# Kernel tuning notes

Hardware: AMD Instinct MI355X
Metric: run time of the kernel (lower is better)

## Reference

```python
import jax, jax.numpy as jnp
import numpy as np

N_NODES = 50000
N_EDGES = 800000
NUM_GRAPHS = 128
FEAT = 128
HID = 64
NUM_LAYERS = 3
OUT = 2
K = 30
LATENT = HID * NUM_LAYERS + 1  # 193 = conv1 kernel size & stride


def _lin(k, i, o):
    s = 1.0 / np.sqrt(i)
    return jax.random.uniform(k, (i, o), jnp.float32, -s, s)


def setup_inputs() -> dict:
    key = jax.random.key(0)
    ks = jax.random.split(key, 16)
    x = jax.random.normal(ks[0], (N_NODES, FEAT), jnp.float32)
    edge_index = jax.random.randint(ks[1], (2, N_EDGES), 0, N_NODES, dtype=jnp.int64)
    batch = jnp.sort(jax.random.randint(ks[2], (N_NODES,), 0, NUM_GRAPHS, dtype=jnp.int64))
    w0 = _lin(ks[3], FEAT, HID); b0 = jnp.zeros((HID,), jnp.float32)
    w1 = _lin(ks[4], HID, HID);  b1 = jnp.zeros((HID,), jnp.float32)
    w2 = _lin(ks[5], HID, HID);  b2 = jnp.zeros((HID,), jnp.float32)
    w3 = _lin(ks[6], HID, 1);    b3 = jnp.zeros((1,), jnp.float32)
    conv1_w = jax.random.normal(ks[7], (16, 1, LATENT), jnp.float32) * (1.0 / np.sqrt(LATENT))
    conv1_b = jnp.zeros((16,), jnp.float32)
    conv2_w = jax.random.normal(ks[8], (32, 16, 5), jnp.float32) * (1.0 / np.sqrt(16 * 5))
    conv2_b = jnp.zeros((32,), jnp.float32)
    dense_dim = (int((K - 2) / 2 + 1) - 5 + 1) * 32  # 352
    lin1_w = _lin(ks[9], dense_dim, 256); lin1_b = jnp.zeros((256,), jnp.float32)
    lin2_w = _lin(ks[10], 256, OUT);      lin2_b = jnp.zeros((OUT,), jnp.float32)
    return dict(x=x, edge_index=edge_index, batch=batch,
                w0=w0, b0=b0, w1=w1, b1=b1, w2=w2, b2=b2, w3=w3, b3=b3,
                conv1_w=conv1_w, conv1_b=conv1_b, conv2_w=conv2_w, conv2_b=conv2_b,
                lin1_w=lin1_w, lin1_b=lin1_b, lin2_w=lin2_w, lin2_b=lin2_b)


def _gcn(h_in, w, b, src, dst, norm, n):
    # GCNConv: out_i = sum_j d_i^-1/2 d_j^-1/2 (x_j W) over A+I, plus bias
    h = h_in @ w
    msg = h[src] * norm[:, None]  # gather over edges (incl. self loops)
    return jax.ops.segment_sum(msg, dst, num_segments=n) + b


def _sort_pool(x, batch, k, g):
    # per-graph descending sort on last channel, top-k, zero-pad
    n, d = x.shape
    order = jnp.lexsort((-x[:, -1], batch))  # primary: batch asc, secondary: last feat desc
    xs, bs = x[order], batch[order]
    counts = jax.ops.segment_sum(jnp.ones((n,), jnp.int32), batch, num_segments=g)
    starts = jnp.cumsum(counts) - counts
    rank = jnp.arange(n) - starts[bs]
    slot = jnp.where(rank < k, rank, k)  # overflow nodes dumped in slot k (discarded)
    out = jnp.zeros((g, k + 1, d), x.dtype).at[bs, slot].set(xs)
    return out[:, :k].reshape(g, k * d)


def _conv1d(z, w, stride):
    return jax.lax.conv_general_dilated(z, w, window_strides=(stride,), padding='VALID',
                                        dimension_numbers=('NCH', 'OIH', 'NCH'))


def reference(x, edge_index, batch, w0, b0, w1, b1, w2, b2, w3, b3,
              conv1_w, conv1_b, conv2_w, conv2_b, lin1_w, lin1_b, lin2_w, lin2_b):
    n = x.shape[0]
    loop = jnp.arange(n, dtype=edge_index.dtype)
    src = jnp.concatenate([edge_index[0], loop])
    dst = jnp.concatenate([edge_index[1], loop])
    deg = jax.ops.segment_sum(jnp.ones_like(src, jnp.float32), dst, num_segments=n)
    dinv = jnp.where(deg > 0, jax.lax.rsqrt(deg), 0.0)
    norm = dinv[src] * dinv[dst]

    h1 = jnp.tanh(_gcn(x,  w0, b0, src, dst, norm, n))
    h2 = jnp.tanh(_gcn(h1, w1, b1, src, dst, norm, n))
    h3 = jnp.tanh(_gcn(h2, w2, b2, src, dst, norm, n))
    h4 = jnp.tanh(_gcn(h3, w3, b3, src, dst, norm, n))
    hcat = jnp.concatenate([h1, h2, h3, h4], axis=-1)  # [N, 193]

    p = _sort_pool(hcat, batch, K, NUM_GRAPHS)  # [G, K*193]
    z = p[:, None, :]                                   # [G, 1, K*193]
    z = jax.nn.relu(_conv1d(z, conv1_w, LATENT) + conv1_b[None, :, None])  # [G,16,K]
    g, c, l = z.shape
    z = z.reshape(g, c, l // 2, 2).max(axis=-1)         # MaxPool1d(2,2) -> [G,16,15]
    z = jax.nn.relu(_conv1d(z, conv2_w, 1) + conv2_b[None, :, None])       # [G,32,11]
    z = z.reshape(g, -1)                                # [G,352]
    z = jax.nn.relu(z @ lin1_w + lin1_b)
    # dropout is identity in eval mode
    return z @ lin2_w + lin2_b
```

## Files before the change

### kernel.cpp

```cpp
#include <hip/hip_runtime.h>
#include <math.h>

#define NGRAPH 128
#define KTOP 30
#define LATENT 193
#define HID 64

typedef unsigned short u16;

__global__ void k_zero(int* edeg, int n) {
    int i = blockIdx.x * blockDim.x + threadIdx.x;
    if (i < n) edeg[i] = 0;
}

__global__ __launch_bounds__(256) void k_gemm_hist(
        const float* __restrict__ A, const float* __restrict__ W,
        float* __restrict__ Hs, int M, int K, int NG,
        const int* __restrict__ dst, const int* __restrict__ batch,
        int* edeg, u16* __restrict__ rank, int* starts,
        int E, int n) {
    __shared__ float As[64][17];
    __shared__ float Bs[16][65];
    int bid = blockIdx.x;
    int gemm_id = (bid % 5 == 0) ? bid / 5 : -1;
    if (gemm_id >= 0 && gemm_id < NG) {
        int tid = threadIdx.x;
        int tx = tid & 15, ty = tid >> 4;
        int br = gemm_id * 64;
        float c[4][4] = {};
        for (int k0 = 0; k0 < K; k0 += 16) {
            {
                int idx = tid * 4;
                int r = idx >> 4;
                int kk = idx & 15;
                int grow = br + r;
                float4 v = make_float4(0.f, 0.f, 0.f, 0.f);
                if (grow < M) v = *(const float4*)(A + (size_t)grow * K + k0 + kk);
                As[r][kk + 0] = v.x; As[r][kk + 1] = v.y;
                As[r][kk + 2] = v.z; As[r][kk + 3] = v.w;
            }
            {
                int idx = tid * 4;
                int kk = idx >> 6;
                int col = idx & 63;
                float4 v = *(const float4*)(W + (size_t)(k0 + kk) * 64 + col);
                Bs[kk][col + 0] = v.x; Bs[kk][col + 1] = v.y;
                Bs[kk][col + 2] = v.z; Bs[kk][col + 3] = v.w;
            }
            __syncthreads();
#pragma unroll
            for (int kk = 0; kk < 16; ++kk) {
                float a[4], b[4];
#pragma unroll
                for (int i = 0; i < 4; i++) a[i] = As[ty + i * 16][kk];
#pragma unroll
                for (int j = 0; j < 4; j++) b[j] = Bs[kk][tx + j * 16];
#pragma unroll
                for (int i = 0; i < 4; i++)
#pragma unroll
                    for (int j = 0; j < 4; j++) c[i][j] += a[i] * b[j];
            }
            __syncthreads();
        }
#pragma unroll
        for (int i = 0; i < 4; i++) {
            int row = br + ty + i * 16;
            if (row >= M) continue;
#pragma unroll
            for (int j = 0; j < 4; j++) {
                int col = tx + j * 16;
                Hs[(size_t)row * HID + col] = c[i][j];
            }
        }
    } else {
        int ngb = min((bid + 4) / 5, NG);
        int fid = bid - ngb;
        int gi = fid * 256 + threadIdx.x;
        if (gi < n) {
            int b = batch[gi];
            if (gi == 0) {
                for (int g = 0; g <= b; g++) starts[g] = 0;
            } else {
                int pb = batch[gi - 1];
                for (int g = pb + 1; g <= b; g++) starts[g] = gi;
            }
            if (gi == n - 1) {
                for (int g = b + 1; g <= NGRAPH; g++) starts[g] = n;
            }
        }
        if (gi < E) {
            int d = dst[gi];
            rank[gi] = (u16)atomicAdd(&edeg[d], 1);
        }
    }
}

__global__ void k_scan1(const int* __restrict__ edeg, int* offs, int* bsum,
                        float* dinv, int n) {
    __shared__ int s[256];
    int t = threadIdx.x;
    int gi = blockIdx.x * 256 + t;
    int v = (gi < n) ? edeg[gi] : 0;
    if (gi < n) dinv[gi] = rsqrtf((float)(v + 1));
    s[t] = v;
    __syncthreads();
    for (int o = 1; o < 256; o <<= 1) {
        int add = (t >= o) ? s[t - o] : 0;
        __syncthreads();
        s[t] += add;
        __syncthreads();
    }
    if (gi < n) offs[gi] = s[t] - v;
    if (t == 255) bsum[blockIdx.x] = s[255];
}

__global__ void k_scan23(int* offs, const int* __restrict__ bsum,
                         int n, int E, int nb) {
    __shared__ int s[256];
    int t = threadIdx.x;
    int bid = blockIdx.x;
    int v = (t < nb) ? bsum[t] : 0;
    s[t] = v;
    __syncthreads();
    for (int o = 1; o < 256; o <<= 1) {
        int add = (t >= o) ? s[t - o] : 0;
        __syncthreads();
        s[t] += add;
        __syncthreads();
    }
    int boffv = (bid == 0) ? 0 : s[bid - 1];
    int gi = bid * 256 + t;
    if (gi < n) offs[gi] += boffv;
    if (gi == 0) offs[n] = E;
}

__global__ __launch_bounds__(256) void k_fill(const int* __restrict__ src,
                                              const int* __restrict__ dst,
                                              const u16* __restrict__ rank,
                                              const int* __restrict__ offs,
                                              u16* __restrict__ csr, int E) {
    int t = blockIdx.x * 256 + threadIdx.x;
    int e0 = t * 4;
    if (e0 + 4 <= E) {
        int4 s4 = *(const int4*)(src + e0);
        int4 d4 = *(const int4*)(dst + e0);
        const u16* rp = rank + e0;
        csr[offs[d4.x] + rp[0]] = (u16)s4.x;
        csr[offs[d4.y] + rp[1]] = (u16)s4.y;
        csr[offs[d4.z] + rp[2]] = (u16)s4.z;
        csr[offs[d4.w] + rp[3]] = (u16)s4.w;
    } else {
        for (int e = e0; e < E; e++)
            csr[offs[dst[e]] + rank[e]] = (u16)src[e];
    }
}

__global__ __launch_bounds__(256) void k_gemm(const float* __restrict__ A,
                                              const float* __restrict__ W,
                                              const float* __restrict__ dinv,
                                              float* __restrict__ Hs,
                                              int M, int K) {
    __shared__ float As[64][17];
    __shared__ float Bs[16][65];
    int tid = threadIdx.x;
    int tx = tid & 15, ty = tid >> 4;
    int br = blockIdx.x * 64;
    float c[4][4] = {};
    for (int k0 = 0; k0 < K; k0 += 16) {
        {
            int idx = tid * 4;
            int r = idx >> 4;
            int kk = idx & 15;
            int grow = br + r;
            float4 v = make_float4(0.f, 0.f, 0.f, 0.f);
            if (grow < M) v = *(const float4*)(A + (size_t)grow * K + k0 + kk);
            As[r][kk + 0] = v.x; As[r][kk + 1] = v.y;
            As[r][kk + 2] = v.z; As[r][kk + 3] = v.w;
        }
        {
            int idx = tid * 4;
            int kk = idx >> 6;
            int col = idx & 63;
            float4 v = *(const float4*)(W + (size_t)(k0 + kk) * 64 + col);
            Bs[kk][col + 0] = v.x; Bs[kk][col + 1] = v.y;
            Bs[kk][col + 2] = v.z; Bs[kk][col + 3] = v.w;
        }
        __syncthreads();
#pragma unroll
        for (int kk = 0; kk < 16; ++kk) {
            float a[4], b[4];
#pragma unroll
            for (int i = 0; i < 4; i++) a[i] = As[ty + i * 16][kk];
#pragma unroll
            for (int j = 0; j < 4; j++) b[j] = Bs[kk][tx + j * 16];
#pragma unroll
            for (int i = 0; i < 4; i++)
#pragma unroll
                for (int j = 0; j < 4; j++) c[i][j] += a[i] * b[j];
        }
        __syncthreads();
    }
#pragma unroll
    for (int i = 0; i < 4; i++) {
        int row = br + ty + i * 16;
        if (row >= M) continue;
        float d = dinv[row];
#pragma unroll
        for (int j = 0; j < 4; j++) {
            int col = tx + j * 16;
            Hs[(size_t)row * HID + col] = c[i][j] * d;
        }
    }
}

template <bool DEFER, bool FUSE_TS>
__global__ __launch_bounds__(256) void k_agg(const float* __restrict__ Hs,
                                             const u16* __restrict__ csr,
                                             const int* __restrict__ offs,
                                             const float* __restrict__ dinv,
                                             const float* __restrict__ b,
                                             float* __restrict__ H, int n,
                                             const float* __restrict__ w3,
                                             float* __restrict__ ts) {
    int wid = threadIdx.x >> 6;
    int lane = threadIdx.x & 63;
    int node = blockIdx.x * 4 + wid;
    if (node >= n) return;
    float d = dinv[node];
    float acc = Hs[(size_t)node * HID + lane];
    if (DEFER) acc *= d;
    int s = offs[node], e = offs[node + 1];
    int i = s;
    for (; i + 8 <= e; i += 8) {
        float part = 0.f;
#pragma unroll
        for (int k = 0; k < 8; k++) {
            int u = csr[i + k];
            float v = Hs[(size_t)u * HID + lane];
            if (DEFER) v *= dinv[u];
            part += v;
        }
        acc += part;
    }
    for (; i < e; i++) {
        int u = csr[i];
        float v = Hs[(size_t)u * HID + lane];
        if (DEFER) v *= dinv[u];
        acc += v;
    }
    float h = tanhf(acc * d + b[lane]);
    H[(size_t)node * HID + lane] = h;
    if (FUSE_TS) {
        float v = h * w3[lane];
        for (int o = 32; o > 0; o >>= 1) v += __shfl_down(v, o, 64);
        if (lane == 0) ts[node] = v * d;
    }
}

__global__ void k_agg4(const float* __restrict__ ts, const u16* __restrict__ csr,
                       const int* __restrict__ offs, const float* __restrict__ dinv,
                       const float* __restrict__ b3, float* h4, int n) {
    int node = blockIdx.x * blockDim.x + threadIdx.x;
    if (node >= n) return;
    float acc = ts[node];
    int s = offs[node], e = offs[node + 1];
    for (int i = s; i < e; i++) acc += ts[csr[i]];
    h4[node] = tanhf(acc * dinv[node] + b3[0]);
}

__global__ __launch_bounds__(1024) void k_select_tail(
        const float* __restrict__ h1, const float* __restrict__ h2,
        const float* __restrict__ h3, const float* __restrict__ h4,
        const int* __restrict__ starts,
        const float* __restrict__ c1w, const float* __restrict__ c1b,
        const float* __restrict__ c2w, const float* __restrict__ c2b,
        const float* __restrict__ l1w, const float* __restrict__ l1b,
        const float* __restrict__ l2w, const float* __restrict__ l2b,
        float* __restrict__ out) {
    __shared__ float p[KTOP * LATENT];
    __shared__ float w1s[16 * LATENT];
    __shared__ float w2s[32 * 16 * 5];
    __shared__ float vv[1024];
    __shared__ int   sel_s[KTOP];
    __shared__ float z1[16 * KTOP];
    __shared__ float z1p[16 * 15];
    __shared__ float flat[352];
    __shared__ float part[1024];
    __shared__ float y1[256];
    int g = blockIdx.x;
    int t = threadIdx.x;
    int s = starts[g], c = starts[g + 1] - s;

    for (int i = t; i < 16 * LATENT; i += 1024) w1s[i] = c1w[i];
    for (int i = t; i < 32 * 16 * 5; i += 1024) w2s[i] = c2w[i];
    if (t < KTOP) sel_s[t] = -1;

    if (c <= 1024) {
        for (int i = t; i < c; i += 1024) vv[i] = h4[s + i];
        __syncthreads();
        for (int i = t; i < c; i += 1024) {
            float vi = vv[i];
            int r = 0;
            for (int j = 0; j < c; j++) {
                float vj = vv[j];
                r += (vj > vi) || (vj == vi && j < i);
            }
            if (r < KTOP) sel_s[r] = s + i;
        }
    } else {
        __syncthreads();
        for (int i = t; i < c; i += 1024) {
            float vi = h4[s + i];
            int r = 0;
            for (int j = 0; j < c; j++) {
                float vj = h4[s + j];
                r += (vj > vi) || (vj == vi && j < i);
            }
            if (r < KTOP) sel_s[r] = s + i;
        }
    }
    __syncthreads();

    for (int i = t; i < KTOP * LATENT; i += 1024) {
        int slot = i / LATENT;
        int j = i - slot * LATENT;
        int node = sel_s[slot];
        float v = 0.f;
        if (node >= 0) {
            if (j < 64)       v = h1[(size_t)node * HID + j];
            else if (j < 128) v = h2[(size_t)node * HID + j - 64];
            else if (j < 192) v = h3[(size_t)node * HID + j - 128];
            else              v = h4[node];
        }
        p[i] = v;
    }
    __syncthreads();
    if (t < 16 * KTOP) {
        int ch = t / KTOP, tt = t - ch * KTOP;
        float sa = c1b[ch];
        const float* wp = &w1s[ch * LATENT];
        const float* pp = &p[tt * LATENT];
        for (int j = 0; j < LATENT; j++) sa += pp[j] * wp[j];
        z1[ch * KTOP + tt] = fmaxf(sa, 0.f);
    }
    __syncthreads();
    if (t < 16 * 15) {
        int ch = t / 15, tt = t - ch * 15;
        z1p[t] = fmaxf(z1[ch * KTOP + 2 * tt], z1[ch * KTOP + 2 * tt + 1]);
    }
    __syncthreads();
    if (t < 32 * 11) {
        int c2 = t / 11, tt = t - c2 * 11;
        float sa = c2b[c2];
        for (int c1i = 0; c1i < 16; c1i++) {
            const float* wp = &w2s[(c2 * 16 + c1i) * 5];
            const float* zp = &z1p[c1i * 15 + tt];
#pragma unroll
            for (int dt = 0; dt < 5; dt++) sa += zp[dt] * wp[dt];
        }
        flat[c2 * 11 + tt] = fmaxf(sa, 0.f);
    }
    __syncthreads();
    {
        int o = t & 255, ch = t >> 8;
        int i0 = ch * 88, i1 = i0 + 88;
        float sa = 0.f;
        for (int i = i0; i < i1; i++) sa += flat[i] * l1w[(size_t)i * 256 + o];
        part[t] = sa;
    }
    __syncthreads();
    if (t < 256)
        y1[t] = fmaxf(part[t] + part[256 + t] + part[512 + t] + part[768 + t] + l1b[t], 0.f);
    __syncthreads();
    if (t < 128) {
        int o = t >> 6, lane = t & 63;
        float sa = 0.f;
        for (int i = lane; i < 256; i += 64) sa += y1[i] * l2w[(size_t)i * 2 + o];
        for (int off = 32; off > 0; off >>= 1) sa += __shfl_down(sa, off, 64);
        if (lane == 0) out[g * 2 + o] = sa + l2b[o];
    }
}

static inline char* align256(char* p) {
    return (char*)(((uintptr_t)p + 255) & ~(uintptr_t)255);
}

extern "C" void kernel_launch(void* const* d_in, const int* in_sizes, int n_in,
                              void* d_out, int out_size, void* d_ws, size_t ws_size,
                              hipStream_t stream) {
    const float* x     = (const float*)d_in[0];
    const int*  eidx   = (const int*)d_in[1];
    const int*  batch  = (const int*)d_in[2];
    const float* w0    = (const float*)d_in[3];
    const float* b0    = (const float*)d_in[4];
    const float* w1    = (const float*)d_in[5];
    const float* b1    = (const float*)d_in[6];
    const float* w2    = (const float*)d_in[7];
    const float* b2    = (const float*)d_in[8];
    const float* w3    = (const float*)d_in[9];
    const float* b3    = (const float*)d_in[10];
    const float* c1w   = (const float*)d_in[11];
    const float* c1b   = (const float*)d_in[12];
    const float* c2w   = (const float*)d_in[13];
    const float* c2b   = (const float*)d_in[14];
    const float* l1w   = (const float*)d_in[15];
    const float* l1b   = (const float*)d_in[16];
    const float* l2w   = (const float*)d_in[17];
    const float* l2b   = (const float*)d_in[18];

    int N = in_sizes[2];
    int E = in_sizes[1] / 2;
    int K0 = in_sizes[0] / N;
    const int* esrc = eidx;
    const int* edst = eidx + E;

    char* w = (char*)d_ws;
    float* dinv  = (float*)w;             w = align256(w + (size_t)N * 4);
    int*   edeg  = (int*)w;               w = align256(w + (size_t)N * 4);
    int*   offs  = (int*)w;               w = align256(w + (size_t)(N + 1) * 4);
    int*   bsum  = (int*)w;               w = align256(w + 1024);
    float* ts    = (float*)w;             w = align256(w + (size_t)N * 4);
    float* h4    = (float*)w;             w = align256(w + (size_t)N * 4);
    int* starts  = (int*)w;               w = align256(w + (NGRAPH + 1) * 4);
    u16* rank    = (u16*)w;               w = align256(w + (size_t)E * 2);
    u16* csr     = (u16*)w;               w = align256(w + (size_t)E * 2);
    float* Hs    = (float*)w;             w = align256(w + (size_t)N * HID * 4);
    float* h1    = (float*)w;             w = align256(w + (size_t)N * HID * 4);
    float* h2    = (float*)w;             w = align256(w + (size_t)N * HID * 4);
    float* h3    = (float*)w;             w = align256(w + (size_t)N * HID * 4);

    int nb = (N + 255) / 256;
    int NG = (N + 63) / 64;
    int NH = (E + 255) / 256;
    int agg_grid = (N + 3) / 4;

    k_zero<<<nb, 256, 0, stream>>>(edeg, N);

    k_gemm_hist<<<NG + NH, 256, 0, stream>>>(x, w0, Hs, N, K0, NG,
                                             edst, batch, edeg, rank, starts, E, N);

    k_scan1<<<nb, 256, 0, stream>>>(edeg, offs, bsum, dinv, N);
    k_scan23<<<nb, 256, 0, stream>>>(offs, bsum, N, E, nb);

    k_fill<<<(E / 4 + 255) / 256 + 1, 256, 0, stream>>>(esrc, edst, rank, offs, csr, E);

    k_agg<true, false><<<agg_grid, 256, 0, stream>>>(Hs, csr, offs, dinv, b0, h1, N, nullptr, nullptr);
    k_gemm<<<NG, 256, 0, stream>>>(h1, w1, dinv, Hs, N, HID);
    k_agg<false, false><<<agg_grid, 256, 0, stream>>>(Hs, csr, offs, dinv, b1, h2, N, nullptr, nullptr);
    k_gemm<<<NG, 256, 0, stream>>>(h2, w2, dinv, Hs, N, HID);
    k_agg<false, true><<<agg_grid, 256, 0, stream>>>(Hs, csr, offs, dinv, b2, h3, N, w3, ts);
    k_agg4<<<nb, 256, 0, stream>>>(ts, csr, offs, dinv, b3, h4, N);

    k_select_tail<<<NGRAPH, 1024, 0, stream>>>(h1, h2, h3, h4, starts,
                                               c1w, c1b, c2w, c2b,
                                               l1w, l1b, l2w, l2b,
                                               (float*)d_out);
}
```

Before: 273.3 us.

## Rework GEMM tile for vector LDS access; coarsen histogram blocks and rank loads

Result: faster. 252.5 us (-7.6%).

```diff
diff --git a/kernel.cpp b/kernel.cpp
--- a/kernel.cpp
+++ b/kernel.cpp
@@ -11,6 +11,62 @@
 __global__ void k_zero(int* edeg, int n) {
     int i = blockIdx.x * blockDim.x + threadIdx.x;
     if (i < n) edeg[i] = 0;
+}
+
+template <bool SCALE>
+__device__ __forceinline__ void gemm_tile(const float* __restrict__ A,
+                                          const float* __restrict__ W,
+                                          const float* __restrict__ dinv,
+                                          float* __restrict__ Hs,
+                                          int M, int K, int br,
+                                          float (*As)[68], float (*Bs)[68]) {
+    int tid = threadIdx.x;
+    int tx = tid & 15, ty = tid >> 4;
+    int kA = (tid & 7) * 4;
+    int rA = tid >> 3;
+    int kB = tid >> 3;
+    int cB = (tid & 7) * 8;
+    float c[4][4] = {};
+    for (int k0 = 0; k0 < K; k0 += 32) {
+#pragma unroll
+        for (int it = 0; it < 2; ++it) {
+            int row = it * 32 + rA;
+            int grow = br + row;
+            float4 v = make_float4(0.f, 0.f, 0.f, 0.f);
+            if (grow < M) v = *(const float4*)(A + (size_t)grow * K + k0 + kA);
+            As[kA + 0][row] = v.x;
+            As[kA + 1][row] = v.y;
+            As[kA + 2][row] = v.z;
+            As[kA + 3][row] = v.w;
+        }
+        {
+            const float* wp = W + (size_t)(k0 + kB) * 64 + cB;
+            float4 v0 = *(const float4*)(wp);
+            float4 v1 = *(const float4*)(wp + 4);
+            *(float4*)&Bs[kB][cB] = v0;
+            *(float4*)&Bs[kB][cB + 4] = v1;
+        }
+        __syncthreads();
+#pragma unroll
+        for (int kk = 0; kk < 32; ++kk) {
+            float4 a4 = *(const float4*)&As[kk][ty * 4];
+            float4 b4 = *(const float4*)&Bs[kk][tx * 4];
+            c[0][0] += a4.x * b4.x; c[0][1] += a4.x * b4.y; c[0][2] += a4.x * b4.z; c[0][3] += a4.x * b4.w;
+            c[1][0] += a4.y * b4.x; c[1][1] += a4.y * b4.y; c[1][2] += a4.y * b4.z; c[1][3] += a4.y * b4.w;
+            c[2][0] += a4.z * b4.x; c[2][1] += a4.z * b4.y; c[2][2] += a4.z * b4.z; c[2][3] += a4.z * b4.w;
+            c[3][0] += a4.w * b4.x; c[3][1] += a4.w * b4.y; c[3][2] += a4.w * b4.z; c[3][3] += a4.w * b4.w;
+        }
+        __syncthreads();
+    }
+#pragma unroll
+    for (int i = 0; i < 4; i++) {
+        int row = br + ty * 4 + i;
+        if (row >= M) continue;
+        float d = SCALE ? dinv[row] : 1.f;
+        float4 o;
+        o.x = c[i][0] * d; o.y = c[i][1] * d; o.z = c[i][2] * d; o.w = c[i][3] * d;
+        *(float4*)(Hs + (size_t)row * HID + tx * 4) = o;
+    }
 }
 
 __global__ __launch_bounds__(256) void k_gemm_hist(
@@ -18,64 +74,19 @@
         float* __restrict__ Hs, int M, int K, int NG,
         const int* __restrict__ dst, const int* __restrict__ batch,
         int* edeg, u16* __restrict__ rank, int* starts,
-        int E, int n) {
-    __shared__ float As[64][17];
-    __shared__ float Bs[16][65];
+        int E, int n, int NH) {
+    __shared__ float As[32][68];
+    __shared__ float Bs[32][68];
     int bid = blockIdx.x;
-    int gemm_id = (bid % 5 == 0) ? bid / 5 : -1;
-    if (gemm_id >= 0 && gemm_id < NG) {
-        int tid = threadIdx.x;
-        int tx = tid & 15, ty = tid >> 4;
-        int br = gemm_id * 64;
-        float c[4][4] = {};
-        for (int k0 = 0; k0 < K; k0 += 16) {
-            {
-                int idx = tid * 4;
-                int r = idx >> 4;
-                int kk = idx & 15;
-                int grow = br + r;
-                float4 v = make_float4(0.f, 0.f, 0.f, 0.f);
-                if (grow < M) v = *(const float4*)(A + (size_t)grow * K + k0 + kk);
-                As[r][kk + 0] = v.x; As[r][kk + 1] = v.y;
-                As[r][kk + 2] = v.z; As[r][kk + 3] = v.w;
-            }
-            {
-                int idx = tid * 4;
-                int kk = idx >> 6;
-                int col = idx & 63;
-                float4 v = *(const float4*)(W + (size_t)(k0 + kk) * 64 + col);
-                Bs[kk][col + 0] = v.x; Bs[kk][col + 1] = v.y;
-                Bs[kk][col + 2] = v.z; Bs[kk][col + 3] = v.w;
-            }
-            __syncthreads();
-#pragma unroll
-            for (int kk = 0; kk < 16; ++kk) {
-                float a[4], b[4];
-#pragma unroll
-                for (int i = 0; i < 4; i++) a[i] = As[ty + i * 16][kk];
-#pragma unroll
-                for (int j = 0; j < 4; j++) b[j] = Bs[kk][tx + j * 16];
-#pragma unroll
-                for (int i = 0; i < 4; i++)
-#pragma unroll
-                    for (int j = 0; j < 4; j++) c[i][j] += a[i] * b[j];
-            }
-            __syncthreads();
-        }
-#pragma unroll
-        for (int i = 0; i < 4; i++) {
-            int row = br + ty + i * 16;
-            if (row >= M) continue;
-#pragma unroll
-            for (int j = 0; j < 4; j++) {
-                int col = tx + j * 16;
-                Hs[(size_t)row * HID + col] = c[i][j];
-            }
-        }
+    if ((bid & 1) == 0) {
+        int gid = bid >> 1;
+        if (gid >= NG) return;
+        gemm_tile<false>(A, W, nullptr, Hs, M, K, gid * 64, As, Bs);
     } else {
-        int ngb = min((bid + 4) / 5, NG);
-        int fid = bid - ngb;
-        int gi = fid * 256 + threadIdx.x;
+        int fid = bid >> 1;
+        if (fid >= NH) return;
+        int t = threadIdx.x;
+        int gi = fid * 256 + t;
         if (gi < n) {
             int b = batch[gi];
             if (gi == 0) {
@@ -88,9 +99,14 @@
                 for (int g = b + 1; g <= NGRAPH; g++) starts[g] = n;
             }
         }
-        if (gi < E) {
-            int d = dst[gi];
-            rank[gi] = (u16)atomicAdd(&edeg[d], 1);
+        int base = fid * 1024;
+#pragma unroll
+        for (int k = 0; k < 4; k++) {
+            int e = base + k * 256 + t;
+            if (e < E) {
+                int d = dst[e];
+                rank[e] = (u16)atomicAdd(&edeg[d], 1);
+            }
         }
     }
 }
@@ -144,11 +160,11 @@
     if (e0 + 4 <= E) {
         int4 s4 = *(const int4*)(src + e0);
         int4 d4 = *(const int4*)(dst + e0);
-        const u16* rp = rank + e0;
-        csr[offs[d4.x] + rp[0]] = (u16)s4.x;
-        csr[offs[d4.y] + rp[1]] = (u16)s4.y;
-        csr[offs[d4.z] + rp[2]] = (u16)s4.z;
-        csr[offs[d4.w] + rp[3]] = (u16)s4.w;
+        uint2 rv = *(const uint2*)(rank + e0);
+        csr[offs[d4.x] + (rv.x & 0xffff)] = (u16)s4.x;
+        csr[offs[d4.y] + (rv.x >> 16)]    = (u16)s4.y;
+        csr[offs[d4.z] + (rv.y & 0xffff)] = (u16)s4.z;
+        csr[offs[d4.w] + (rv.y >> 16)]    = (u16)s4.w;
     } else {
         for (int e = e0; e < E; e++)
             csr[offs[dst[e]] + rank[e]] = (u16)src[e];
@@ -160,57 +176,9 @@
                                               const float* __restrict__ dinv,
                                               float* __restrict__ Hs,
                                               int M, int K) {
-    __shared__ float As[64][17];
-    __shared__ float Bs[16][65];
-    int tid = threadIdx.x;
-    int tx = tid & 15, ty = tid >> 4;
-    int br = blockIdx.x * 64;
-    float c[4][4] = {};
-    for (int k0 = 0; k0 < K; k0 += 16) {
-        {
-            int idx = tid * 4;
-            int r = idx >> 4;
-            int kk = idx & 15;
-            int grow = br + r;
-            float4 v = make_float4(0.f, 0.f, 0.f, 0.f);
-            if (grow < M) v = *(const float4*)(A + (size_t)grow * K + k0 + kk);
-            As[r][kk + 0] = v.x; As[r][kk + 1] = v.y;
-            As[r][kk + 2] = v.z; As[r][kk + 3] = v.w;
-        }
-        {
-            int idx = tid * 4;
-            int kk = idx >> 6;
-            int col = idx & 63;
-            float4 v = *(const float4*)(W + (size_t)(k0 + kk) * 64 + col);
-            Bs[kk][col + 0] = v.x; Bs[kk][col + 1] = v.y;
-            Bs[kk][col + 2] = v.z; Bs[kk][col + 3] = v.w;
-        }
-        __syncthreads();
-#pragma unroll
-        for (int kk = 0; kk < 16; ++kk) {
-            float a[4], b[4];
-#pragma unroll
-            for (int i = 0; i < 4; i++) a[i] = As[ty + i * 16][kk];
-#pragma unroll
-            for (int j = 0; j < 4; j++) b[j] = Bs[kk][tx + j * 16];
-#pragma unroll
-            for (int i = 0; i < 4; i++)
-#pragma unroll
-                for (int j = 0; j < 4; j++) c[i][j] += a[i] * b[j];
-        }
-        __syncthreads();
-    }
-#pragma unroll
-    for (int i = 0; i < 4; i++) {
-        int row = br + ty + i * 16;
-        if (row >= M) continue;
-        float d = dinv[row];
-#pragma unroll
-        for (int j = 0; j < 4; j++) {
-            int col = tx + j * 16;
-            Hs[(size_t)row * HID + col] = c[i][j] * d;
-        }
-    }
+    __shared__ float As[32][68];
+    __shared__ float Bs[32][68];
+    gemm_tile<true>(A, W, dinv, Hs, M, K, blockIdx.x * 64, As, Bs);
 }
 
 template <bool DEFER, bool FUSE_TS>
@@ -431,13 +399,14 @@
 
     int nb = (N + 255) / 256;
     int NG = (N + 63) / 64;
-    int NH = (E + 255) / 256;
+    int NH = (E + 1023) / 1024;
     int agg_grid = (N + 3) / 4;
 
     k_zero<<<nb, 256, 0, stream>>>(edeg, N);
 
-    k_gemm_hist<<<NG + NH, 256, 0, stream>>>(x, w0, Hs, N, K0, NG,
-                                             edst, batch, edeg, rank, starts, E, N);
+    int g1 = 2 * (NG > NH ? NG : NH);
+    k_gemm_hist<<<g1, 256, 0, stream>>>(x, w0, Hs, N, K0, NG,
+                                        edst, batch, edeg, rank, starts, E, N, NH);
 
     k_scan1<<<nb, 256, 0, stream>>>(edeg, offs, bsum, dinv, N);
     k_scan23<<<nb, 256, 0, stream>>>(offs, bsum, N, E, nb);
```
